# Kernel optimization log

Hardware: AMD Instinct MI355X
Metric: run time of the kernel (lower is better)

The kernel has to match this reference:

```python
import jax, jax.numpy as jnp
import numpy as np

LAM = 0.5
B, N, C = 512, 197, 384


def _mlp(x, w1, b1, w2, b2):
    # Linear -> exact GELU -> Linear (dropout is identity in eval)
    h = jax.nn.gelu(x @ w1 + b1, approximate=False)
    return h @ w2 + b2


def _ln(x, g, b, eps=1e-5):
    m = jnp.mean(x, axis=-1, keepdims=True)
    v = jnp.mean((x - m) ** 2, axis=-1, keepdims=True)
    return (x - m) * jax.lax.rsqrt(v + eps) * g + b


def _l2norm(x, eps=1e-12):
    n = jnp.sqrt(jnp.sum(x * x, axis=-1, keepdims=True))
    return x / jnp.maximum(n, eps)


def setup_inputs() -> dict:
    key = jax.random.key(0)
    ks = iter(jax.random.split(key, 40))
    s = 0.02

    def w(shape):
        return (jax.random.normal(next(ks), shape, jnp.float32) * s)

    inp = {
        'feat_query': jax.random.normal(next(ks), (B, N, C), jnp.float32),
        'feat_shot': jax.random.normal(next(ks), (B, N, C), jnp.float32),
        'feat_query_start': jax.random.normal(next(ks), (B, N, C), jnp.float32),
        'feat_shot_start': jax.random.normal(next(ks), (B, N, C), jnp.float32),
        # fc1: 384 -> 96 -> 384
        'fc1_w1': w((384, 96)), 'fc1_b1': jnp.zeros((96,)),
        'fc1_w2': w((96, 384)), 'fc1_b2': jnp.zeros((384,)),
        'ln1_g': jnp.ones((384,)), 'ln1_b': jnp.zeros((384,)),
        # fc3: 196 -> 128 -> 196
        'fc3_w1': w((196, 128)), 'fc3_b1': jnp.zeros((128,)),
        'fc3_w2': w((128, 196)), 'fc3_b2': jnp.zeros((196,)),
        'ln3_g': jnp.ones((196,)), 'ln3_b': jnp.zeros((196,)),
        # fc4: 384 -> 96 -> 384
        'fc4_w1': w((384, 96)), 'fc4_b1': jnp.zeros((96,)),
        'fc4_w2': w((96, 384)), 'fc4_b2': jnp.zeros((384,)),
        'ln4_g': jnp.ones((384,)), 'ln4_b': jnp.zeros((384,)),
        # fc2: 9604 -> 256 -> 1
        'fc2_w1': w((98 * 98, 256)), 'fc2_b1': jnp.zeros((256,)),
        'fc2_w2': w((256, 1)), 'fc2_b2': jnp.zeros((1,)),
        # cosine_sim.layer1: 384 -> 96 -> 384
        'cs_w1': w((384, 96)), 'cs_b1': jnp.zeros((96,)),
        'cs_w2': w((96, 384)), 'cs_b2': jnp.zeros((384,)),
    }
    return inp


def reference(feat_query, feat_shot, feat_query_start, feat_shot_start,
              fc1_w1, fc1_b1, fc1_w2, fc1_b2, ln1_g, ln1_b,
              fc3_w1, fc3_b1, fc3_w2, fc3_b2, ln3_g, ln3_b,
              fc4_w1, fc4_b1, fc4_w2, fc4_b2, ln4_g, ln4_b,
              fc2_w1, fc2_b1, fc2_w2, fc2_b2,
              cs_w1, cs_b1, cs_w2, cs_b2):
    def fc1_res(x):  # Mlp over mean token, added back (broadcast over seq)
        m = jnp.mean(x, axis=1, keepdims=True)  # [B,1,C]
        return _ln(_mlp(m, fc1_w1, fc1_b1, fc1_w2, fc1_b2) + x, ln1_g, ln1_b)

    fq = fc1_res(feat_query)
    fs = fc1_res(feat_shot)
    fqs = fc1_res(feat_query_start)
    fss = fc1_res(feat_shot_start)

    query_class = fq[:, 0:1, :]          # [B,1,384]
    query_image = fq[:, 1:, :]           # [B,196,384]
    query_image_start = fqs[:, 1:, :]
    support_class = fs[:, 0:1, :]
    support_image = fs[:, 1:, :]
    support_image_start = fss[:, 1:, :]

    def fc3_path(x):  # Mlp over token dim (196) + LN(196)
        xt = jnp.swapaxes(x, -1, -2)     # [B,384,196]
        xt = _ln(_mlp(xt, fc3_w1, fc3_b1, fc3_w2, fc3_b2), ln3_g, ln3_b)
        return jnp.swapaxes(xt, -1, -2)

    query_image_start = fc3_path(query_image_start)
    support_image_start = fc3_path(support_image_start)

    query_image = _ln(_mlp(query_image * query_image_start, fc4_w1, fc4_b1, fc4_w2, fc4_b2), ln4_g, ln4_b)
    support_image = _ln(_mlp(support_image * support_image_start, fc4_w1, fc4_b1, fc4_w2, fc4_b2), ln4_g, ln4_b)

    fq2 = query_image + LAM * query_class
    fs2 = support_image + LAM * support_class
    fq2 = _l2norm(fq2)
    fq2 = fq2 - jnp.mean(fq2, axis=2, keepdims=True)
    fs2 = _l2norm(fs2)
    fs2 = fs2 - jnp.mean(fs2, axis=2, keepdims=True)

    out = jnp.einsum('bqc,bsc->bqs', fq2, fs2)        # [B,196,196]
    b = out.shape[0]
    out = out.reshape(b, 98, 2, 98, 2).mean(axis=(2, 4))  # AvgPool2d(2,2)
    out = out.reshape(b, 98 * 98)
    out = (_mlp_fc2(out ** 2, fc2_w1, fc2_b1, fc2_w2, fc2_b2)).squeeze(-1)  # [B]

    # Cosine_Sim on class tokens
    qx = _mlp(query_class[:, 0, :], cs_w1, cs_b1, cs_w2, cs_b2)
    sy = _mlp(support_class[:, 0, :], cs_w1, cs_b1, cs_w2, cs_b2)
    eps = 1e-8
    cosine = jnp.sum(qx * sy, axis=-1) / (
        jnp.maximum(jnp.linalg.norm(qx, axis=-1), eps) * jnp.maximum(jnp.linalg.norm(sy, axis=-1), eps))

    return out, cosine, query_class, support_class


def _mlp_fc2(x, w1, b1, w2, b2):
    h = jax.nn.gelu(x @ w1 + b1, approximate=False)
    return h @ w2 + b2
```

## Files before the change

kernel.cpp:

```cpp
#include <hip/hip_runtime.h>
#include <math.h>

typedef unsigned short ushort_t;
typedef __attribute__((ext_vector_type(8))) short bf16x8;
typedef __attribute__((ext_vector_type(4))) float f32x4;

__device__ __forceinline__ float geluf(float x){
  return 0.5f*x*(1.0f+erff(x*0.70710678118654752440f));
}
__device__ __forceinline__ float bfu(unsigned int u){
  union { unsigned int i; float f; } v; v.i = (u & 0xffffu) << 16; return v.f;
}
__device__ __forceinline__ unsigned int f2b(float f){
  union { float f; unsigned int i; } v; v.f = f;
  unsigned int r = v.i + 0x7fffu + ((v.i >> 16) & 1u);
  return (r >> 16);
}


__global__ __launch_bounds__(384) void k_mean(
    const float* __restrict__ x0, const float* __restrict__ x1,
    const float* __restrict__ x2, const float* __restrict__ x3,
    float* __restrict__ meanb){
  int s = blockIdx.x >> 9, b = blockIdx.x & 511, c = threadIdx.x;
  const float* x = (s==0)?x0:(s==1)?x1:(s==2)?x2:x3;
  const float* p = x + ((size_t)b*197)*384 + c;
  float acc = 0.f;
  #pragma unroll 4
  for (int t=0;t<197;++t) acc += p[(size_t)t*384];
  meanb[((size_t)s*512+b)*384+c] = acc*(1.0f/197.0f);
}

__global__ __launch_bounds__(384) void k_fc1(
    const float* __restrict__ meanb, const float* __restrict__ w1,
    const float* __restrict__ b1, const float* __restrict__ w2,
    const float* __restrict__ b2, float* __restrict__ mlp1){
  __shared__ float ms[384];
  __shared__ float hs[96];
  int row = blockIdx.x, tid = threadIdx.x;
  ms[tid] = meanb[(size_t)row*384 + tid];
  __syncthreads();
  if (tid < 96){
    float a = b1[tid];
    for (int c=0;c<384;++c) a += ms[c]*w1[c*96+tid];
    hs[tid] = geluf(a);
  }
  __syncthreads();
  float a = b2[tid];
  for (int j=0;j<96;++j) a += hs[j]*w2[j*384+tid];
  mlp1[(size_t)row*384 + tid] = a;
}

__global__ __launch_bounds__(256) void k_stats(
    const float* __restrict__ x0, const float* __restrict__ x1,
    const float* __restrict__ x2, const float* __restrict__ x3,
    const float* __restrict__ mlp1, float* __restrict__ mu, float* __restrict__ rstd){
  int sb = blockIdx.x;
  int s = sb >> 9, b = sb & 511;
  const float* x = (s==0)?x0:(s==1)?x1:(s==2)?x2:x3;
  const float* mp = mlp1 + (size_t)sb*384;
  int tid = threadIdx.x, w = tid >> 6, lane = tid & 63;
  int g = lane >> 4, il = lane & 15;
  float4 mreg[6];
  #pragma unroll
  for (int it = 0; it < 6; ++it)
    mreg[it] = *reinterpret_cast<const float4*>(&mp[il*4 + 64*it]);
  for (int t0 = 0; t0 < 208; t0 += 16){
    int t = t0 + w*4 + g;
    if (t < 197){
      const float* xp = x + ((size_t)b*197 + t)*384 + il*4;
      float sum = 0.f, sq = 0.f;
      #pragma unroll
      for (int it = 0; it < 6; ++it){
        float4 v = *reinterpret_cast<const float4*>(xp + 64*it);
        float a0 = v.x + mreg[it].x, a1 = v.y + mreg[it].y;
        float a2 = v.z + mreg[it].z, a3 = v.w + mreg[it].w;
        sum += a0+a1+a2+a3;
        sq  += a0*a0+a1*a1+a2*a2+a3*a3;
      }
      #pragma unroll
      for (int o=1;o<16;o<<=1){ sum += __shfl_xor(sum,o); sq += __shfl_xor(sq,o); }
      if (il == 0){
        int row = sb*197 + t;
        float m = sum*(1.0f/384.0f);
        mu[row] = m;
        rstd[row] = rsqrtf(sq*(1.0f/384.0f) - m*m + 1e-5f);
      }
    }
  }
}

__global__ __launch_bounds__(384) void k_class(
    const float* __restrict__ x0, const float* __restrict__ x1,
    const float* __restrict__ mlp1, const float* __restrict__ mu,
    const float* __restrict__ rstd, const float* __restrict__ g1,
    const float* __restrict__ bb1, float* __restrict__ dout){
  int s = blockIdx.x >> 9, b = blockIdx.x & 511, c = threadIdx.x;
  const float* x = s ? x1 : x0;
  int srow = (s*512 + b)*197;
  float v = x[((size_t)b*197)*384 + c] + mlp1[((size_t)s*512+b)*384 + c];
  float y = (v - mu[srow])*rstd[srow]*g1[c] + bb1[c];
  dout[1024 + (size_t)s*196608 + (size_t)b*384 + c] = y;
}

__global__ __launch_bounds__(384) void k_cosine(
    const float* __restrict__ w1, const float* __restrict__ b1,
    const float* __restrict__ w2, const float* __restrict__ b2,
    float* __restrict__ dout){
  __shared__ float qrow[384], srw[384], hq[96], hs[96];
  __shared__ float rd0[384], rd1[384], rd2[384];
  int b = blockIdx.x, tid = threadIdx.x;
  qrow[tid] = dout[1024   + (size_t)b*384 + tid];
  srw[tid]  = dout[197632 + (size_t)b*384 + tid];
  __syncthreads();
  if (tid < 96){
    float a = b1[tid];
    for (int c=0;c<384;++c) a += qrow[c]*w1[c*96+tid];
    hq[tid] = geluf(a);
  } else if (tid < 192){
    int j = tid - 96;
    float a = b1[j];
    for (int c=0;c<384;++c) a += srw[c]*w1[c*96+j];
    hs[j] = geluf(a);
  }
  __syncthreads();
  float qx = b2[tid], sy = b2[tid];
  for (int j=0;j<96;++j){ qx += hq[j]*w2[j*384+tid]; sy += hs[j]*w2[j*384+tid]; }
  rd0[tid] = qx*sy; rd1[tid] = qx*qx; rd2[tid] = sy*sy;
  __syncthreads();
  if (tid < 64){
    float d=0.f,nq=0.f,ns=0.f;
    for (int i=tid;i<384;i+=64){ d+=rd0[i]; nq+=rd1[i]; ns+=rd2[i]; }
    #pragma unroll
    for (int o=32;o;o>>=1){ d+=__shfl_down(d,o); nq+=__shfl_down(nq,o); ns+=__shfl_down(ns,o); }
    if (tid==0) dout[512 + b] = d / (fmaxf(sqrtf(nq),1e-8f)*fmaxf(sqrtf(ns),1e-8f));
  }
}

__global__ __launch_bounds__(256) void k_wt(
    const float* __restrict__ w1_4, const float* __restrict__ w2_4,
    const float* __restrict__ w1_3, const float* __restrict__ w2_3,
    ushort_t* __restrict__ w1t, ushort_t* __restrict__ w2t,
    ushort_t* __restrict__ w1t3, ushort_t* __restrict__ w2t3){
  int idx = blockIdx.x*256 + threadIdx.x;
  if (idx < 36864){
    int c = idx / 96, j = idx - c*96;
    w2t[idx] = (ushort_t)f2b(w2_4[(size_t)j*384 + c]);
  } else if (idx < 73728){
    int k = idx - 36864;
    int j = k / 384, c = k - j*384;
    w1t[k] = (ushort_t)f2b(w1_4[(size_t)c*96 + j]);
  } else if (idx < 102400){
    int k = idx - 73728;
    int j = k / 224, t = k - j*224;
    w1t3[k] = (t < 196) ? (ushort_t)f2b(w1_3[(size_t)t*128 + j]) : (ushort_t)0;
  } else {
    int k = idx - 102400;
    int tp = k / 128, j = k - tp*128;
    w2t3[k] = (tp < 196) ? (ushort_t)f2b(w2_3[(size_t)j*196 + tp]) : (ushort_t)0;
  }
}

__global__ __launch_bounds__(256) void k_fc3(
    const float* __restrict__ x,
    const float* __restrict__ m1_base,
    const float* __restrict__ mu_s,
    const float* __restrict__ rstd_s,
    const float* __restrict__ g1, const float* __restrict__ bln1,
    const ushort_t* __restrict__ w1t3,
    const float* __restrict__ b1,
    const ushort_t* __restrict__ w2t3,
    const float* __restrict__ b2, const float* __restrict__ g3,
    const float* __restrict__ b3,
    ushort_t* __restrict__ Qout){
  __shared__ ushort_t Xs[64][232];
  __shared__ float m1s[64], g1s[64], b1s[64];
  __shared__ float mus[196], rss[196];
  __shared__ float b1j[128];
  __shared__ float b2s[208], g3s[208], b3s[208];
  int bid = blockIdx.x;
  int b = bid/6, c0 = (bid%6)*64;
  int tid = threadIdx.x;
  if (tid < 64){
    m1s[tid] = m1_base[(size_t)b*384 + c0 + tid];
    g1s[tid] = g1[c0+tid]; b1s[tid] = bln1[c0+tid];
  }
  if (tid < 128) b1j[tid] = b1[tid];
  if (tid < 196){ mus[tid] = mu_s[b*197 + tid + 1]; rss[tid] = rstd_s[b*197 + tid + 1]; }
  if (tid < 208){
    float bb=0.f, gg=0.f, b3v=0.f;
    if (tid < 196){ bb = b2[tid]; gg = g3[tid]; b3v = b3[tid]; }
    b2s[tid]=bb; g3s[tid]=gg; b3s[tid]=b3v;
  }
  for (int i = tid; i < 64*14; i += 256){
    *reinterpret_cast<unsigned int*>(&Xs[i/14][196 + 2*(i%14)]) = 0u;
  }
  __syncthreads();
  for (int e = 0; e < 7; ++e){
    int idx = e*256 + tid;
    if (idx < 1568){
      int t2 = idx >> 4, c4 = idx & 15;
      int t0 = t2*2;
      const float* xr = &x[((size_t)b*197 + t0 + 1)*384 + c0 + c4*4];
      float4 xv0 = *reinterpret_cast<const float4*>(xr);
      float4 xv1 = *reinterpret_cast<const float4*>(xr + 384);
      float mu0 = mus[t0], rs0 = rss[t0], mu1 = mus[t0+1], rs1 = rss[t0+1];
      int c = c4*4;
      unsigned int u0 = f2b(((xv0.x + m1s[c+0]) - mu0)*rs0*g1s[c+0] + b1s[c+0])
                      | (f2b(((xv1.x + m1s[c+0]) - mu1)*rs1*g1s[c+0] + b1s[c+0]) << 16);
      unsigned int u1 = f2b(((xv0.y + m1s[c+1]) - mu0)*rs0*g1s[c+1] + b1s[c+1])
                      | (f2b(((xv1.y + m1s[c+1]) - mu1)*rs1*g1s[c+1] + b1s[c+1]) << 16);
      unsigned int u2 = f2b(((xv0.z + m1s[c+2]) - mu0)*rs0*g1s[c+2] + b1s[c+2])
                      | (f2b(((xv1.z + m1s[c+2]) - mu1)*rs1*g1s[c+2] + b1s[c+2]) << 16);
      unsigned int u3 = f2b(((xv0.w + m1s[c+3]) - mu0)*rs0*g1s[c+3] + b1s[c+3])
                      | (f2b(((xv1.w + m1s[c+3]) - mu1)*rs1*g1s[c+3] + b1s[c+3]) << 16);
      *reinterpret_cast<unsigned int*>(&Xs[c+0][t0]) = u0;
      *reinterpret_cast<unsigned int*>(&Xs[c+1][t0]) = u1;
      *reinterpret_cast<unsigned int*>(&Xs[c+2][t0]) = u2;
      *reinterpret_cast<unsigned int*>(&Xs[c+3][t0]) = u3;
    }
  }
  __syncthreads();
  int w = tid >> 6, lane = tid & 63;
  int cl = lane & 15, kg = lane >> 4;
  f32x4 hacc[8];
  #pragma unroll
  for (int jf=0;jf<8;++jf){ f32x4 z={0.f,0.f,0.f,0.f}; hacc[jf]=z; }
  const ushort_t* zrow = &Xs[w*16 + cl][kg*8];
  for (int kc = 0; kc < 7; ++kc){
    bf16x8 xb = *reinterpret_cast<const bf16x8*>(zrow + kc*32);
    #pragma unroll
    for (int jf=0;jf<8;++jf){
      const ushort_t* ap = w1t3 + (size_t)(jf*16 + cl)*224 + kg*8 + kc*32;
      hacc[jf] = __builtin_amdgcn_mfma_f32_16x16x32_bf16(
          *reinterpret_cast<const bf16x8*>(ap), xb, hacc[jf], 0, 0, 0);
    }
  }
  #pragma unroll
  for (int jf=0;jf<8;++jf){
    f32x4 y = hacc[jf];
    int j0 = jf*16 + kg*4;
    uint2 pk;
    pk.x = f2b(geluf(y[0]+b1j[j0+0])) | (f2b(geluf(y[1]+b1j[j0+1]))<<16);
    pk.y = f2b(geluf(y[2]+b1j[j0+2])) | (f2b(geluf(y[3]+b1j[j0+3]))<<16);
    *reinterpret_cast<uint2*>(&Xs[w*16 + cl][j0]) = pk;
  }
  f32x4 yacc[13];
  #pragma unroll
  for (int tf=0;tf<13;++tf){ f32x4 z={0.f,0.f,0.f,0.f}; yacc[tf]=z; }
  const ushort_t* hrow = &Xs[w*16 + cl][kg*8];
  for (int kc = 0; kc < 4; ++kc){
    bf16x8 hb = *reinterpret_cast<const bf16x8*>(hrow + kc*32);
    #pragma unroll
    for (int tf=0;tf<13;++tf){
      const ushort_t* bp = w2t3 + (size_t)(tf*16 + cl)*128 + kg*8 + kc*32;
      yacc[tf] = __builtin_amdgcn_mfma_f32_16x16x32_bf16(
          hb, *reinterpret_cast<const bf16x8*>(bp), yacc[tf], 0, 0, 0);
    }
  }
  float sum0=0.f,sum1=0.f,sum2=0.f,sum3=0.f, sq0=0.f,sq1=0.f,sq2=0.f,sq3=0.f;
  #pragma unroll
  for (int tf=0;tf<13;++tf){
    int tp = tf*16 + cl;
    float bb = b2s[tp];
    f32x4 y = yacc[tf];
    y[0]+=bb; y[1]+=bb; y[2]+=bb; y[3]+=bb;
    yacc[tf] = y;
    sum0+=y[0]; sum1+=y[1]; sum2+=y[2]; sum3+=y[3];
    sq0+=y[0]*y[0]; sq1+=y[1]*y[1]; sq2+=y[2]*y[2]; sq3+=y[3]*y[3];
  }
  #pragma unroll
  for (int o=1;o<16;o<<=1){
    sum0+=__shfl_xor(sum0,o); sum1+=__shfl_xor(sum1,o);
    sum2+=__shfl_xor(sum2,o); sum3+=__shfl_xor(sum3,o);
    sq0+=__shfl_xor(sq0,o); sq1+=__shfl_xor(sq1,o);
    sq2+=__shfl_xor(sq2,o); sq3+=__shfl_xor(sq3,o);
  }
  float m0=sum0*(1.0f/196.0f), m1v=sum1*(1.0f/196.0f), m2=sum2*(1.0f/196.0f), m3=sum3*(1.0f/196.0f);
  float r0=rsqrtf(sq0*(1.0f/196.0f)-m0*m0+1e-5f);
  float r1=rsqrtf(sq1*(1.0f/196.0f)-m1v*m1v+1e-5f);
  float r2=rsqrtf(sq2*(1.0f/196.0f)-m2*m2+1e-5f);
  float r3=rsqrtf(sq3*(1.0f/196.0f)-m3*m3+1e-5f);
  int cbase = c0 + w*16 + kg*4;
  #pragma unroll
  for (int tf=0;tf<13;++tf){
    int tp = tf*16 + cl;
    if (tp < 196){
      float gg = g3s[tp], bb3 = b3s[tp];
      f32x4 y = yacc[tf];
      unsigned int o0 = f2b((y[0]-m0)*r0*gg + bb3);
      unsigned int o1 = f2b((y[1]-m1v)*r1*gg + bb3);
      unsigned int o2 = f2b((y[2]-m2)*r2*gg + bb3);
      unsigned int o3 = f2b((y[3]-m3)*r3*gg + bb3);
      uint2 pk; pk.x = o0 | (o1<<16); pk.y = o2 | (o3<<16);
      *reinterpret_cast<uint2*>(&Qout[((size_t)b*196 + tp)*384 + cbase]) = pk;
    }
  }
}

__global__ __launch_bounds__(256) void k_fc4a(
    const float* __restrict__ x,
    const float* __restrict__ m1_base,
    const float* __restrict__ mu_s,
    const float* __restrict__ rstd_s,
    const float* __restrict__ g1, const float* __restrict__ bln1,
    const ushort_t* __restrict__ Qin,
    const ushort_t* __restrict__ w1t,
    const float* __restrict__ b1mlp,
    ushort_t* __restrict__ h4s){
  __shared__ ushort_t Zs[64][392];
  __shared__ float m1s[384], g1s[384], b1s[384];
  __shared__ float mus[64], rss[64];
  __shared__ float b1m[96];
  int bid = blockIdx.x;
  int b = bid >> 2, tt0 = (bid & 3)*64;
  int tid = threadIdx.x;
  const float* m1 = m1_base + (size_t)b*384;
  for (int i = tid; i < 384; i += 256){ m1s[i] = m1[i]; g1s[i] = g1[i]; b1s[i] = bln1[i]; }
  if (tid < 96) b1m[tid] = b1mlp[tid];
  if (tid < 64){
    int t = tt0 + tid; int tc = t < 196 ? t : 195;
    mus[tid] = mu_s[b*197 + tc + 1]; rss[tid] = rstd_s[b*197 + tc + 1];
  }
  __syncthreads();
  for (int e = 0; e < 24; ++e){
    int v = e*256 + tid;
    int row = v/96, col4 = v - row*96;
    int t = tt0 + row; int tc = t < 196 ? t : 195;
    float valid = (t < 196) ? 1.f : 0.f;
    float4 xv = *reinterpret_cast<const float4*>(&x[((size_t)b*197 + tc + 1)*384 + col4*4]);
    uint2 qv = *reinterpret_cast<const uint2*>(&Qin[((size_t)b*196 + tc)*384 + col4*4]);
    float muv = mus[row], rsv = rss[row];
    int c = col4*4;
    float z0 = (((xv.x + m1s[c+0]) - muv)*rsv*g1s[c+0] + b1s[c+0]) * bfu(qv.x)      * valid;
    float z1 = (((xv.y + m1s[c+1]) - muv)*rsv*g1s[c+1] + b1s[c+1]) * bfu(qv.x>>16)  * valid;
    float z2 = (((xv.z + m1s[c+2]) - muv)*rsv*g1s[c+2] + b1s[c+2]) * bfu(qv.y)      * valid;
    float z3 = (((xv.w + m1s[c+3]) - muv)*rsv*g1s[c+3] + b1s[c+3]) * bfu(qv.y>>16)  * valid;
    uint2 pk; pk.x = f2b(z0) | (f2b(z1)<<16); pk.y = f2b(z2) | (f2b(z3)<<16);
    *reinterpret_cast<uint2*>(&Zs[row][col4*4]) = pk;
  }
  __syncthreads();
  int w = tid >> 6, lane = tid & 63;
  int tr = tt0 + w*16 + (lane & 15);
  int kg = lane >> 4;
  f32x4 acc0 = {0.f,0.f,0.f,0.f}, acc1 = {0.f,0.f,0.f,0.f}, acc2 = {0.f,0.f,0.f,0.f};
  f32x4 acc3 = {0.f,0.f,0.f,0.f}, acc4 = {0.f,0.f,0.f,0.f}, acc5 = {0.f,0.f,0.f,0.f};
  const ushort_t* arow = w1t + (size_t)(lane & 15)*384 + kg*8;
  const ushort_t* zrow = &Zs[w*16 + (lane & 15)][kg*8];
  for (int kc = 0; kc < 12; ++kc){
    bf16x8 zb = *reinterpret_cast<const bf16x8*>(zrow + kc*32);
    bf16x8 a0 = *reinterpret_cast<const bf16x8*>(arow + kc*32);
    bf16x8 a1 = *reinterpret_cast<const bf16x8*>(arow + kc*32 + 16*384);
    bf16x8 a2 = *reinterpret_cast<const bf16x8*>(arow + kc*32 + 32*384);
    bf16x8 a3 = *reinterpret_cast<const bf16x8*>(arow + kc*32 + 48*384);
    bf16x8 a4 = *reinterpret_cast<const bf16x8*>(arow + kc*32 + 64*384);
    bf16x8 a5 = *reinterpret_cast<const bf16x8*>(arow + kc*32 + 80*384);
    acc0 = __builtin_amdgcn_mfma_f32_16x16x32_bf16(a0, zb, acc0, 0, 0, 0);
    acc1 = __builtin_amdgcn_mfma_f32_16x16x32_bf16(a1, zb, acc1, 0, 0, 0);
    acc2 = __builtin_amdgcn_mfma_f32_16x16x32_bf16(a2, zb, acc2, 0, 0, 0);
    acc3 = __builtin_amdgcn_mfma_f32_16x16x32_bf16(a3, zb, acc3, 0, 0, 0);
    acc4 = __builtin_amdgcn_mfma_f32_16x16x32_bf16(a4, zb, acc4, 0, 0, 0);
    acc5 = __builtin_amdgcn_mfma_f32_16x16x32_bf16(a5, zb, acc5, 0, 0, 0);
  }
  if (tr < 196){
    ushort_t* dst = h4s + ((size_t)b*196 + tr)*96 + kg*4;
    #pragma unroll
    for (int jb = 0; jb < 6; ++jb){
      f32x4 y = (jb==0)?acc0:(jb==1)?acc1:(jb==2)?acc2:(jb==3)?acc3:(jb==4)?acc4:acc5;
      int j0 = jb*16 + kg*4;
      uint2 pk;
      pk.x = f2b(geluf(y[0]+b1m[j0+0])) | (f2b(geluf(y[1]+b1m[j0+1]))<<16);
      pk.y = f2b(geluf(y[2]+b1m[j0+2])) | (f2b(geluf(y[3]+b1m[j0+3]))<<16);
      *reinterpret_cast<uint2*>(dst + jb*16) = pk;
    }
  }
}

__global__ __launch_bounds__(256) void k_fc4b(
    const ushort_t* __restrict__ h4s,
    const ushort_t* __restrict__ w2t,
    const float* __restrict__ b2, const float* __restrict__ g4,
    const float* __restrict__ bb4,
    const float* __restrict__ cls_base,
    ushort_t* __restrict__ Qo){
  __shared__ float b2s[384], g4s[384], b4s[384], cl_s[384];
  int bid = blockIdx.x;
  int b = bid >> 2, ttile = bid & 3;
  int tid = threadIdx.x, w = tid >> 6, lane = tid & 63;
  const float* cls = cls_base + (size_t)b*384;
  for (int i = tid; i < 384; i += 256){
    b2s[i] = b2[i]; g4s[i] = g4[i]; b4s[i] = bb4[i]; cl_s[i] = cls[i];
  }
  __syncthreads();
  int tr = ttile*64 + w*16 + (lane & 15);
  int trc = tr < 196 ? tr : 195;
  int kg = lane >> 4;
  const ushort_t* hp = h4s + ((size_t)b*196 + trc)*96 + kg*8;
  bf16x8 hb0 = *reinterpret_cast<const bf16x8*>(hp);
  bf16x8 hb1 = *reinterpret_cast<const bf16x8*>(hp + 32);
  bf16x8 hb2 = *reinterpret_cast<const bf16x8*>(hp + 64);
  const ushort_t* ap_base = w2t + (size_t)(lane & 15)*96 + kg*8;
  f32x4 acc[24];
  #pragma unroll
  for (int af = 0; af < 24; ++af){
    const ushort_t* ap = ap_base + (size_t)af*16*96;
    bf16x8 a0 = *reinterpret_cast<const bf16x8*>(ap);
    bf16x8 a1 = *reinterpret_cast<const bf16x8*>(ap + 32);
    bf16x8 a2 = *reinterpret_cast<const bf16x8*>(ap + 64);
    f32x4 z = {0.f,0.f,0.f,0.f};
    z = __builtin_amdgcn_mfma_f32_16x16x32_bf16(a0, hb0, z, 0, 0, 0);
    z = __builtin_amdgcn_mfma_f32_16x16x32_bf16(a1, hb1, z, 0, 0, 0);
    z = __builtin_amdgcn_mfma_f32_16x16x32_bf16(a2, hb2, z, 0, 0, 0);
    acc[af] = z;
  }
  float sum = 0.f, sq = 0.f;
  #pragma unroll
  for (int af = 0; af < 24; ++af){
    int cb = af*16 + kg*4;
    float4 bv = *reinterpret_cast<const float4*>(&b2s[cb]);
    f32x4 y = acc[af];
    y[0] += bv.x; y[1] += bv.y; y[2] += bv.z; y[3] += bv.w;
    acc[af] = y;
    sum += y[0]+y[1]+y[2]+y[3];
    sq  += y[0]*y[0]+y[1]*y[1]+y[2]*y[2]+y[3]*y[3];
  }
  sum += __shfl_xor(sum, 16); sum += __shfl_xor(sum, 32);
  sq  += __shfl_xor(sq, 16);  sq  += __shfl_xor(sq, 32);
  float m4 = sum*(1.0f/384.0f);
  float rs = rsqrtf(sq*(1.0f/384.0f) - m4*m4 + 1e-5f);
  float s2 = 0.f;
  #pragma unroll
  for (int af = 0; af < 24; ++af){
    int cb = af*16 + kg*4;
    float4 gv = *reinterpret_cast<const float4*>(&g4s[cb]);
    float4 bb = *reinterpret_cast<const float4*>(&b4s[cb]);
    float4 cv = *reinterpret_cast<const float4*>(&cl_s[cb]);
    f32x4 y = acc[af];
    y[0] = (y[0]-m4)*rs*gv.x + bb.x + 0.5f*cv.x;
    y[1] = (y[1]-m4)*rs*gv.y + bb.y + 0.5f*cv.y;
    y[2] = (y[2]-m4)*rs*gv.z + bb.z + 0.5f*cv.z;
    y[3] = (y[3]-m4)*rs*gv.w + bb.w + 0.5f*cv.w;
    acc[af] = y;
    s2 += y[0]*y[0]+y[1]*y[1]+y[2]*y[2]+y[3]*y[3];
  }
  s2 += __shfl_xor(s2, 16); s2 += __shfl_xor(s2, 32);
  float inv = 1.0f/fmaxf(sqrtf(s2), 1e-12f);
  float sm = 0.f;
  #pragma unroll
  for (int af = 0; af < 24; ++af){
    f32x4 y = acc[af];
    y[0]*=inv; y[1]*=inv; y[2]*=inv; y[3]*=inv;
    acc[af] = y;
    sm += y[0]+y[1]+y[2]+y[3];
  }
  sm += __shfl_xor(sm, 16); sm += __shfl_xor(sm, 32);
  sm *= (1.0f/384.0f);
  if (tr < 196){
    ushort_t* dst = Qo + ((size_t)b*196 + tr)*384 + kg*4;
    #pragma unroll
    for (int af = 0; af < 24; ++af){
      f32x4 y = acc[af];
      uint2 pk;
      pk.x = f2b(y[0]-sm) | (f2b(y[1]-sm)<<16);
      pk.y = f2b(y[2]-sm) | (f2b(y[3]-sm)<<16);
      *reinterpret_cast<uint2*>(dst + af*16) = pk;
    }
  }
}

__global__ __launch_bounds__(256) void k_sim(
    const ushort_t* __restrict__ Q, const ushort_t* __restrict__ S,
    float* __restrict__ P){
  int bx = blockIdx.x;
  int b = bx >> 4, qt = (bx >> 2) & 3, st = bx & 3;
  int tid = threadIdx.x;
  int w = tid >> 6, lane = tid & 63;
  int wr = w >> 1, wc = w & 1;
  int q0 = qt*64 + wr*32, s0 = st*64 + wc*32;
  int rrow = lane & 15, kg = lane >> 4;
  const ushort_t* Qb_ = Q + (size_t)b*196*384;
  const ushort_t* Sb_ = S + (size_t)b*196*384;
  int qr0 = min(q0 + rrow, 195), qr1 = min(q0 + 16 + rrow, 195);
  int sr0 = min(s0 + rrow, 195), sr1 = min(s0 + 16 + rrow, 195);
  const ushort_t* qp0 = Qb_ + (size_t)qr0*384 + kg*8;
  const ushort_t* qp1 = Qb_ + (size_t)qr1*384 + kg*8;
  const ushort_t* sp0 = Sb_ + (size_t)sr0*384 + kg*8;
  const ushort_t* sp1 = Sb_ + (size_t)sr1*384 + kg*8;
  f32x4 acc00 = {0.f,0.f,0.f,0.f}, acc01 = {0.f,0.f,0.f,0.f};
  f32x4 acc10 = {0.f,0.f,0.f,0.f}, acc11 = {0.f,0.f,0.f,0.f};
  for (int k0 = 0; k0 < 384; k0 += 32){
    bf16x8 a0 = *reinterpret_cast<const bf16x8*>(qp0 + k0);
    bf16x8 a1 = *reinterpret_cast<const bf16x8*>(qp1 + k0);
    bf16x8 b0 = *reinterpret_cast<const bf16x8*>(sp0 + k0);
    bf16x8 b1 = *reinterpret_cast<const bf16x8*>(sp1 + k0);
    acc00 = __builtin_amdgcn_mfma_f32_16x16x32_bf16(a0, b0, acc00, 0, 0, 0);
    acc01 = __builtin_amdgcn_mfma_f32_16x16x32_bf16(a0, b1, acc01, 0, 0, 0);
    acc10 = __builtin_amdgcn_mfma_f32_16x16x32_bf16(a1, b0, acc10, 0, 0, 0);
    acc11 = __builtin_amdgcn_mfma_f32_16x16x32_bf16(a1, b1, acc11, 0, 0, 0);
  }
  int c = lane & 15, g = lane >> 4;
  float* Pb = P + (size_t)b*98*98;
  #pragma unroll
  for (int i = 0; i < 2; ++i){
    #pragma unroll
    for (int j = 0; j < 2; ++j){
      f32x4 v = (i==0) ? (j==0 ? acc00 : acc01) : (j==0 ? acc10 : acc11);
      float p0 = v[0] + v[1];
      float p1 = v[2] + v[3];
      float t0 = p0 + __shfl_xor(p0, 1);
      float t1 = p1 + __shfl_xor(p1, 1);
      if (!(c & 1)){
        int qp = (q0 + 16*i + 4*g) >> 1;
        int sp = (s0 + 16*j + c) >> 1;
        if (sp < 98){
          if (qp     < 98) Pb[(size_t)(qp    )*98 + sp] = 0.25f*t0;
          if (qp + 1 < 98) Pb[(size_t)(qp + 1)*98 + sp] = 0.25f*t1;
        }
      }
    }
  }
}

__global__ __launch_bounds__(256) void k_fc2a(
    const float* __restrict__ P, const float* __restrict__ w1,
    float* __restrict__ Cpart){
  __shared__ float p2[8][688];
  int bx = blockIdx.x;
  int mb = bx & 63, ks = bx >> 6;
  int b0 = mb*8, k0 = ks*686;
  int tid = threadIdx.x;
  for (int idx = tid; idx < 8*686; idx += 256){
    int r = idx / 686, i = idx - r*686;
    float v = P[(size_t)(b0+r)*9604 + k0 + i];
    p2[r][i] = v*v;
  }
  __syncthreads();
  float acc[8];
  #pragma unroll
  for (int r=0;r<8;++r) acc[r]=0.f;
  for (int ii=0; ii<686; ++ii){
    float w = w1[(size_t)(k0+ii)*256 + tid];
    #pragma unroll
    for (int r=0;r<8;++r) acc[r] += p2[r][ii]*w;
  }
  #pragma unroll
  for (int r=0;r<8;++r) Cpart[((size_t)ks*512 + b0 + r)*256 + tid] = acc[r];
}

__global__ __launch_bounds__(256) void k_fc2b(
    const float* __restrict__ Cpart, const float* __restrict__ b1,
    const float* __restrict__ w2, const float* __restrict__ b2,
    float* __restrict__ outp){
  __shared__ float red[4];
  int b = blockIdx.x, tid = threadIdx.x;
  float s = 0.f;
  for (int ks = 0; ks < 14; ++ks) s += Cpart[((size_t)ks*512 + b)*256 + tid];
  float h = geluf(s + b1[tid]) * w2[tid];
  #pragma unroll
  for (int o=32;o;o>>=1) h += __shfl_down(h,o);
  int w = tid >> 6, lane = tid & 63;
  if (lane==0) red[w] = h;
  __syncthreads();
  if (tid==0) outp[b] = red[0]+red[1]+red[2]+red[3] + b2[0];
}

extern "C" void kernel_launch(void* const* d_in, const int* in_sizes, int n_in,
                              void* d_out, int out_size, void* d_ws, size_t ws_size,
                              hipStream_t stream){
  const float* fq  = (const float*)d_in[0];
  const float* fs  = (const float*)d_in[1];
  const float* fqs = (const float*)d_in[2];
  const float* fss = (const float*)d_in[3];
  const float* fc1_w1 = (const float*)d_in[4];
  const float* fc1_b1 = (const float*)d_in[5];
  const float* fc1_w2 = (const float*)d_in[6];
  const float* fc1_b2 = (const float*)d_in[7];
  const float* ln1_g = (const float*)d_in[8];
  const float* ln1_b = (const float*)d_in[9];
  const float* fc3_w1 = (const float*)d_in[10];
  const float* fc3_b1 = (const float*)d_in[11];
  const float* fc3_w2 = (const float*)d_in[12];
  const float* fc3_b2 = (const float*)d_in[13];
  const float* ln3_g = (const float*)d_in[14];
  const float* ln3_b = (const float*)d_in[15];
  const float* fc4_w1 = (const float*)d_in[16];
  const float* fc4_b1 = (const float*)d_in[17];
  const float* fc4_w2 = (const float*)d_in[18];
  const float* fc4_b2 = (const float*)d_in[19];
  const float* ln4_g = (const float*)d_in[20];
  const float* ln4_b = (const float*)d_in[21];
  const float* fc2_w1 = (const float*)d_in[22];
  const float* fc2_b1 = (const float*)d_in[23];
  const float* fc2_w2 = (const float*)d_in[24];
  const float* fc2_b2 = (const float*)d_in[25];
  const float* cs_w1 = (const float*)d_in[26];
  const float* cs_b1 = (const float*)d_in[27];
  const float* cs_w2 = (const float*)d_in[28];
  const float* cs_b2 = (const float*)d_in[29];
  float* out = (float*)d_out;
  char* ws = (char*)d_ws;
  float* meanb  = (float*)(ws + 0);
  ushort_t* w2t  = (ushort_t*)(ws + 0);
  ushort_t* w1t  = (ushort_t*)(ws + 73728);
  ushort_t* w1t3 = (ushort_t*)(ws + 147456);
  ushort_t* w2t3 = (ushort_t*)(ws + 204800);
  float* mlp1   = (float*)(ws + 3145728);
  float* mu     = (float*)(ws + 6291456);
  float* rstd   = (float*)(ws + 7905280);
  ushort_t* h4  = (ushort_t*)(ws + 9519104);
  float* P      = (float*)(ws + 9519104);
  float* Cpart  = (float*)(ws + 29188096);
  ushort_t* Qb  = (ushort_t*)(ws + 59850752);
  ushort_t* Sb  = (ushort_t*)(ws + 136921088);
  const size_t H4S = (size_t)512*196*96;

  k_mean<<<2048, 384, 0, stream>>>(fq, fs, fqs, fss, meanb);
  k_fc1<<<2048, 384, 0, stream>>>(meanb, fc1_w1, fc1_b1, fc1_w2, fc1_b2, mlp1);
  k_wt<<<504, 256, 0, stream>>>(fc4_w1, fc4_w2, fc3_w1, fc3_w2,
                                w1t, w2t, w1t3, w2t3);
  k_stats<<<2048, 256, 0, stream>>>(fq, fs, fqs, fss, mlp1, mu, rstd);
  k_class<<<1024, 384, 0, stream>>>(fq, fs, mlp1, mu, rstd, ln1_g, ln1_b, out);
  k_cosine<<<512, 384, 0, stream>>>(cs_w1, cs_b1, cs_w2, cs_b2, out);
  k_fc3<<<3072, 256, 0, stream>>>(fqs, mlp1 + (size_t)2*512*384, mu + 2*100864, rstd + 2*100864,
                                  ln1_g, ln1_b, w1t3, fc3_b1, w2t3, fc3_b2, ln3_g, ln3_b, Qb);
  k_fc3<<<3072, 256, 0, stream>>>(fss, mlp1 + (size_t)3*512*384, mu + 3*100864, rstd + 3*100864,
                                  ln1_g, ln1_b, w1t3, fc3_b1, w2t3, fc3_b2, ln3_g, ln3_b, Sb);
  k_fc4a<<<2048, 256, 0, stream>>>(fq, mlp1, mu, rstd, ln1_g, ln1_b,
                                   Qb, w1t, fc4_b1, h4);
  k_fc4a<<<2048, 256, 0, stream>>>(fs, mlp1 + (size_t)512*384, mu + 100864, rstd + 100864,
                                   ln1_g, ln1_b, Sb, w1t, fc4_b1, h4 + H4S);
  k_fc4b<<<2048, 256, 0, stream>>>(h4,       w2t, fc4_b2, ln4_g, ln4_b, out + 1024,          Qb);
  k_fc4b<<<2048, 256, 0, stream>>>(h4 + H4S, w2t, fc4_b2, ln4_g, ln4_b, out + 1024 + 196608, Sb);
  k_sim<<<8192, 256, 0, stream>>>(Qb, Sb, P);
  k_fc2a<<<896, 256, 0, stream>>>(P, fc2_w1, Cpart);
  k_fc2b<<<512, 256, 0, stream>>>(Cpart, fc2_b1, fc2_w2, fc2_b2, out);
}
```

Baseline: 1.475 ms.

## Stage fc3 second-layer weights in LDS and double-buffer first-layer weight loads

In the fc3 kernel, the second MLP layer's weights (w2t3) are now staged into a shared-memory tile in two halves, so the MFMA loop reads B-fragments from LDS instead of global memory. The first-layer A-fragments (w1t3) are software-prefetched one k-chunk ahead into registers, so global load latency overlaps with the MFMAs. The cost is about 30KB of extra LDS, which may reduce occupancy, plus extra __syncthreads barriers and more register pressure from the aC/aN arrays.

```diff
diff --git a/kernel.cpp b/kernel.cpp
--- a/kernel.cpp
+++ b/kernel.cpp
@@ -174,6 +174,7 @@
     const float* __restrict__ b3,
     ushort_t* __restrict__ Qout){
   __shared__ ushort_t Xs[64][232];
+  __shared__ ushort_t W2s[112][136];
   __shared__ float m1s[64], g1s[64], b1s[64];
   __shared__ float mus[196], rss[196];
   __shared__ float b1j[128];
@@ -191,6 +192,11 @@
     float bb=0.f, gg=0.f, b3v=0.f;
     if (tid < 196){ bb = b2[tid]; gg = g3[tid]; b3v = b3[tid]; }
     b2s[tid]=bb; g3s[tid]=gg; b3s[tid]=b3v;
+  }
+  for (int i = tid; i < 112*16; i += 256){
+    int r = i >> 4, q = i & 15;
+    *reinterpret_cast<uint4*>(&W2s[r][q*8]) =
+        *reinterpret_cast<const uint4*>(&w2t3[(size_t)r*128 + q*8]);
   }
   for (int i = tid; i < 64*14; i += 256){
     *reinterpret_cast<unsigned int*>(&Xs[i/14][196 + 2*(i%14)]) = 0u;
@@ -227,14 +233,23 @@
   #pragma unroll
   for (int jf=0;jf<8;++jf){ f32x4 z={0.f,0.f,0.f,0.f}; hacc[jf]=z; }
   const ushort_t* zrow = &Xs[w*16 + cl][kg*8];
+  const ushort_t* abase = w1t3 + (size_t)cl*224 + kg*8;
+  bf16x8 aC[8], aN[8];
+  #pragma unroll
+  for (int jf=0;jf<8;++jf)
+    aC[jf] = *reinterpret_cast<const bf16x8*>(abase + jf*16*224);
   for (int kc = 0; kc < 7; ++kc){
     bf16x8 xb = *reinterpret_cast<const bf16x8*>(zrow + kc*32);
-    #pragma unroll
-    for (int jf=0;jf<8;++jf){
-      const ushort_t* ap = w1t3 + (size_t)(jf*16 + cl)*224 + kg*8 + kc*32;
-      hacc[jf] = __builtin_amdgcn_mfma_f32_16x16x32_bf16(
-          *reinterpret_cast<const bf16x8*>(ap), xb, hacc[jf], 0, 0, 0);
-    }
+    if (kc < 6){
+      #pragma unroll
+      for (int jf=0;jf<8;++jf)
+        aN[jf] = *reinterpret_cast<const bf16x8*>(abase + jf*16*224 + (kc+1)*32);
+    }
+    #pragma unroll
+    for (int jf=0;jf<8;++jf)
+      hacc[jf] = __builtin_amdgcn_mfma_f32_16x16x32_bf16(aC[jf], xb, hacc[jf], 0, 0, 0);
+    #pragma unroll
+    for (int jf=0;jf<8;++jf) aC[jf] = aN[jf];
   }
   #pragma unroll
   for (int jf=0;jf<8;++jf){
@@ -252,8 +267,24 @@
   for (int kc = 0; kc < 4; ++kc){
     bf16x8 hb = *reinterpret_cast<const bf16x8*>(hrow + kc*32);
     #pragma unroll
-    for (int tf=0;tf<13;++tf){
-      const ushort_t* bp = w2t3 + (size_t)(tf*16 + cl)*128 + kg*8 + kc*32;
+    for (int tf=0;tf<7;++tf){
+      const ushort_t* bp = &W2s[tf*16 + cl][kg*8 + kc*32];
+      yacc[tf] = __builtin_amdgcn_mfma_f32_16x16x32_bf16(
+          hb, *reinterpret_cast<const bf16x8*>(bp), yacc[tf], 0, 0, 0);
+    }
+  }
+  __syncthreads();
+  for (int i = tid; i < 96*16; i += 256){
+    int r = i >> 4, q = i & 15;
+    *reinterpret_cast<uint4*>(&W2s[r][q*8]) =
+        *reinterpret_cast<const uint4*>(&w2t3[(size_t)(112 + r)*128 + q*8]);
+  }
+  __syncthreads();
+  for (int kc = 0; kc < 4; ++kc){
+    bf16x8 hb = *reinterpret_cast<const bf16x8*>(hrow + kc*32);
+    #pragma unroll
+    for (int tf=7;tf<13;++tf){
+      const ushort_t* bp = &W2s[tf*16 + cl - 112][kg*8 + kc*32];
       yacc[tf] = __builtin_amdgcn_mfma_f32_16x16x32_bf16(
           hb, *reinterpret_cast<const bf16x8*>(bp), yacc[tf], 0, 0, 0);
     }
```

After: 1.401 ms. 1.05x faster.
